# Kernel optimization log

Measured on AMD Instinct MI355X. Metric: run time of the kernel, lower is better.

## Reference

```python
import jax, jax.numpy as jnp
import numpy as np

B, T, H = 16, 1024, 256
L = 2048
NUM_CLASSES = 100000

def setup_inputs() -> dict:
    key = jax.random.key(0)
    k1, k2, k3 = jax.random.split(key, 3)
    inputs = jax.random.normal(k1, (B, T, H), dtype=jnp.float32)
    labels_selected = jax.random.randint(k2, (B, L), 0, NUM_CLASSES + 1, dtype=jnp.int64)
    attention_table = jax.random.normal(k3, (NUM_CLASSES + 1, H), dtype=jnp.float32) * 0.02
    return {"inputs": inputs, "labels_selected": labels_selected, "attention_table": attention_table}

def reference(inputs, labels_selected, attention_table):
    # Gather label embeddings as queries: (B, L, H)
    attn_weights = attention_table[labels_selected]
    # Unscaled dot-product scores: (B, L, T)
    scores = jnp.einsum('blh,bth->blt', attn_weights, inputs)
    attention = jax.nn.softmax(scores, axis=-1)
    # Weighted sum of inputs: (B, L, H)
    logits = jnp.einsum('blt,bth->blh', attention, inputs)
    return (logits, attention)
```

## Files before the change

kernel.cpp:

```cpp
#include <hip/hip_runtime.h>

#define Bdim 16
#define Tdim 1024
#define Hdim 256
#define Ldim 2048

typedef __attribute__((ext_vector_type(8))) short short8;
typedef __attribute__((ext_vector_type(4))) short short4_t;
typedef __attribute__((ext_vector_type(16))) float floatx16;

__device__ __forceinline__ ushort f2bf(float x) {
    union { float f; unsigned u; } v; v.f = x;
    unsigned r = v.u + 0x7fffu + ((v.u >> 16) & 1u);
    return (ushort)(r >> 16);
}
__device__ __forceinline__ float bf2f(ushort u) {
    union { unsigned u; float f; } v; v.u = ((unsigned)u) << 16;
    return v.f;
}
__device__ __forceinline__ short8 pack8(float4 a, float4 b) {
    short8 r;
    r[0] = (short)f2bf(a.x); r[1] = (short)f2bf(a.y); r[2] = (short)f2bf(a.z); r[3] = (short)f2bf(a.w);
    r[4] = (short)f2bf(b.x); r[5] = (short)f2bf(b.y); r[6] = (short)f2bf(b.z); r[7] = (short)f2bf(b.w);
    return r;
}

__global__ __launch_bounds__(256) void convert_kernel(
    const float* __restrict__ in, ushort* __restrict__ outN, ushort* __restrict__ outT) {
    __shared__ ushort lds[64][68];
    const int b = blockIdx.z, h0 = blockIdx.y * 64, t0 = blockIdx.x * 64;
    const int tid = threadIdx.x;
#pragma unroll
    for (int i = 0; i < 2; i++) {
        const int tt = tid + i * 256;
        const int r = tt >> 3, c = (tt & 7) * 8;
        const float4* src = (const float4*)(in + ((size_t)(b * Tdim + t0 + r)) * Hdim + h0 + c);
        short8 u = pack8(src[0], src[1]);
        *(short8*)(outN + ((size_t)(b * Tdim + t0 + r)) * Hdim + h0 + c) = u;
        short4_t lo = {u[0], u[1], u[2], u[3]}, hi = {u[4], u[5], u[6], u[7]};
        *(short4_t*)&lds[r][c] = lo;
        *(short4_t*)&lds[r][c + 4] = hi;
    }
    __syncthreads();
#pragma unroll
    for (int i = 0; i < 2; i++) {
        const int tt = tid + i * 256;
        const int hh = tt >> 3, c = (tt & 7) * 8;
        short8 u;
#pragma unroll
        for (int j = 0; j < 8; j++) u[j] = (short)lds[c + j][hh];
        *(short8*)(outT + ((size_t)(b * Hdim + h0 + hh)) * Tdim + t0 + c) = u;
    }
}

__global__ __launch_bounds__(512, 4) void attn_kernel(
    const float* __restrict__ table, const int* __restrict__ labels,
    const ushort* __restrict__ kn, const ushort* __restrict__ vt,
    float* __restrict__ logits_out, float* __restrict__ attn_out) {
    __shared__ ushort P[32][1032];
    __shared__ float stats[8][32];
    float* rowinv = &stats[0][0];

    const int bid = blockIdx.x;
    const int xcd = bid & 7, w = bid >> 3;
    const int b = xcd * 2 + (w >> 6);
    const int l0 = (w & 63) * 32;
    const int tid = threadIdx.x;
    const int wave = tid >> 6, lane = tid & 63;
    const int half = lane >> 5, m = lane & 31;

    ushort (*qt)[264] = (ushort(*)[264]) & P[0][0];

    {
        const int row = tid >> 4, cc = (tid & 15) * 16;
        const int lab = labels[b * Ldim + l0 + row];
        const float4* src = (const float4*)(table + (size_t)lab * Hdim + cc);
        float4 f0 = src[0], f1 = src[1], f2 = src[2], f3 = src[3];
        *(short8*)&qt[row][cc] = pack8(f0, f1);
        *(short8*)&qt[row][cc + 8] = pack8(f2, f3);
    }
    __syncthreads();

    floatx16 acc[4];
#pragma unroll
    for (int nt = 0; nt < 4; nt++)
#pragma unroll
        for (int r = 0; r < 16; r++) acc[nt][r] = 0.f;
    {
        const int t0s = wave * 128;
        const ushort* kb = kn + ((size_t)(b * Tdim + t0s + m)) * Hdim + half * 8;
        const ushort* qb = &qt[m][half * 8];
#pragma unroll
        for (int ks = 0; ks < 16; ks++) {
            short8 af = *(const short8*)(qb + ks * 16);
            short8 b0 = *(const short8*)(kb + ks * 16);
            short8 b1 = *(const short8*)(kb + 32 * Hdim + ks * 16);
            short8 b2 = *(const short8*)(kb + 64 * Hdim + ks * 16);
            short8 b3 = *(const short8*)(kb + 96 * Hdim + ks * 16);
            acc[0] = __builtin_amdgcn_mfma_f32_32x32x16_bf16(af, b0, acc[0], 0, 0, 0);
            acc[1] = __builtin_amdgcn_mfma_f32_32x32x16_bf16(af, b1, acc[1], 0, 0, 0);
            acc[2] = __builtin_amdgcn_mfma_f32_32x32x16_bf16(af, b2, acc[2], 0, 0, 0);
            acc[3] = __builtin_amdgcn_mfma_f32_32x32x16_bf16(af, b3, acc[3], 0, 0, 0);
        }
    }

    float rs[16];
#pragma unroll
    for (int nt = 0; nt < 4; nt++)
#pragma unroll
        for (int r = 0; r < 16; r++) {
            float e = __expf(acc[nt][r]);
            acc[nt][r] = e;
            if (nt == 0) rs[r] = e; else rs[r] += e;
        }
#pragma unroll
    for (int s = 1; s < 32; s <<= 1)
#pragma unroll
        for (int r = 0; r < 16; r++) rs[r] += __shfl_xor(rs[r], s, 64);
    if (m == 0) {
#pragma unroll
        for (int r = 0; r < 16; r++) stats[wave][(r & 3) + 8 * (r >> 2) + 4 * half] = rs[r];
    }
    __syncthreads();

    {
        const int t0s = wave * 128;
#pragma unroll
        for (int nt = 0; nt < 4; nt++)
#pragma unroll
            for (int r = 0; r < 16; r++)
                P[(r & 3) + 8 * (r >> 2) + 4 * half][t0s + nt * 32 + m] = f2bf(acc[nt][r]);
    }
    if (tid < 32) {
        float d = 0.f;
#pragma unroll
        for (int wv = 0; wv < 8; wv++) d += stats[wv][tid];
        rowinv[tid] = 1.0f / d;
    }

    const int h0 = wave * 32;
    const ushort* vb = vt + ((size_t)(b * Hdim + h0 + m)) * Tdim + half * 8;
    short8 v0p = *(const short8*)(vb);
    short8 v1p = *(const short8*)(vb + 32 * 16);
    __syncthreads();

#pragma unroll
    for (int r = 0; r < 4; r++) {
        const int row = wave * 4 + r;
        const float inv = rowinv[row];
        const ushort* pr = &P[row][lane * 8];
        float* dst = attn_out + ((size_t)(b * Ldim + l0 + row)) * Tdim + lane * 8;
        short8 u0 = *(const short8*)(pr);
        short8 u1 = *(const short8*)(pr + 512);
        float4 o;
        o.x = bf2f((ushort)u0[0]) * inv; o.y = bf2f((ushort)u0[1]) * inv;
        o.z = bf2f((ushort)u0[2]) * inv; o.w = bf2f((ushort)u0[3]) * inv;
        *(float4*)(dst) = o;
        o.x = bf2f((ushort)u0[4]) * inv; o.y = bf2f((ushort)u0[5]) * inv;
        o.z = bf2f((ushort)u0[6]) * inv; o.w = bf2f((ushort)u0[7]) * inv;
        *(float4*)(dst + 4) = o;
        o.x = bf2f((ushort)u1[0]) * inv; o.y = bf2f((ushort)u1[1]) * inv;
        o.z = bf2f((ushort)u1[2]) * inv; o.w = bf2f((ushort)u1[3]) * inv;
        *(float4*)(dst + 512) = o;
        o.x = bf2f((ushort)u1[4]) * inv; o.y = bf2f((ushort)u1[5]) * inv;
        o.z = bf2f((ushort)u1[6]) * inv; o.w = bf2f((ushort)u1[7]) * inv;
        *(float4*)(dst + 516) = o;
    }

    {
        floatx16 c0, c1;
#pragma unroll
        for (int r = 0; r < 16; r++) { c0[r] = 0.f; c1[r] = 0.f; }
        const ushort* pb = &P[m][half * 8];
#pragma unroll
        for (int ks = 0; ks < 32; ks++) {
            short8 a0 = *(const short8*)(pb + ks * 16);
            short8 v0 = (ks == 0) ? v0p : *(const short8*)(vb + ks * 16);
            c0 = __builtin_amdgcn_mfma_f32_32x32x16_bf16(a0, v0, c0, 0, 0, 0);
            short8 a1 = *(const short8*)(pb + (ks + 32) * 16);
            short8 v1 = (ks == 0) ? v1p : *(const short8*)(vb + (ks + 32) * 16);
            c1 = __builtin_amdgcn_mfma_f32_32x32x16_bf16(a1, v1, c1, 0, 0, 0);
        }
#pragma unroll
        for (int r = 0; r < 16; r++) {
            const int row = (r & 3) + 8 * (r >> 2) + 4 * half;
            logits_out[((size_t)(b * Ldim + l0 + row)) * Hdim + h0 + m] =
                (c0[r] + c1[r]) * rowinv[row];
        }
    }
}

extern "C" void kernel_launch(void* const* d_in, const int* in_sizes, int n_in,
                              void* d_out, int out_size, void* d_ws, size_t ws_size,
                              hipStream_t stream) {
    const float* inputs = (const float*)d_in[0];
    const int* labels   = (const int*)d_in[1];
    const float* table  = (const float*)d_in[2];
    float* out = (float*)d_out;

    ushort* kn = (ushort*)d_ws;
    ushort* vt = kn + (size_t)Bdim * Tdim * Hdim;

    convert_kernel<<<dim3(Tdim / 64, Hdim / 64, Bdim), 256, 0, stream>>>(inputs, kn, vt);

    float* logits_out = out;
    float* attn_out = out + (size_t)Bdim * Ldim * Hdim;
    attn_kernel<<<Bdim * (Ldim / 32), 512, 0, stream>>>(table, labels, kn, vt,
                                                        logits_out, attn_out);
}
```

Measured before the change: 356.1 us.

## Stream P through double-buffered 256-column LDS strips and store attention from registers

Replaces the full 32x1032 bf16 probability tile in LDS with two 32x264 strip buffers that are filled in turn by pairs of waves, with a barrier between strips, during the P·V MFMA loop. The attention output is now written straight from registers (packed bf16 times the row inverse) instead of being re-read from LDS. The aim is to cut LDS use per block so more blocks fit per CU, and to remove the LDS round trip for the attention store. In exchange the kernel has more barriers, holds the packed values in extra registers, and the per-lane strided float stores of attention are less coalesced than the old float4 row writes.

```diff
diff --git a/kernel.cpp b/kernel.cpp
--- a/kernel.cpp
+++ b/kernel.cpp
@@ -57,7 +57,7 @@
     const float* __restrict__ table, const int* __restrict__ labels,
     const ushort* __restrict__ kn, const ushort* __restrict__ vt,
     float* __restrict__ logits_out, float* __restrict__ attn_out) {
-    __shared__ ushort P[32][1032];
+    __shared__ ushort bufs[2][32][264];
     __shared__ float stats[8][32];
     float* rowinv = &stats[0][0];
 
@@ -69,7 +69,7 @@
     const int wave = tid >> 6, lane = tid & 63;
     const int half = lane >> 5, m = lane & 31;
 
-    ushort (*qt)[264] = (ushort(*)[264]) & P[0][0];
+    ushort (*qt)[264] = bufs[0];
 
     {
         const int row = tid >> 4, cc = (tid & 15) * 16;
@@ -123,14 +123,6 @@
     }
     __syncthreads();
 
-    {
-        const int t0s = wave * 128;
-#pragma unroll
-        for (int nt = 0; nt < 4; nt++)
-#pragma unroll
-            for (int r = 0; r < 16; r++)
-                P[(r & 3) + 8 * (r >> 2) + 4 * half][t0s + nt * 32 + m] = f2bf(acc[nt][r]);
-    }
     if (tid < 32) {
         float d = 0.f;
 #pragma unroll
@@ -138,48 +130,68 @@
         rowinv[tid] = 1.0f / d;
     }
 
-    const int h0 = wave * 32;
-    const ushort* vb = vt + ((size_t)(b * Hdim + h0 + m)) * Tdim + half * 8;
-    short8 v0p = *(const short8*)(vb);
-    short8 v1p = *(const short8*)(vb + 32 * 16);
-    __syncthreads();
-
-#pragma unroll
-    for (int r = 0; r < 4; r++) {
-        const int row = wave * 4 + r;
-        const float inv = rowinv[row];
-        const ushort* pr = &P[row][lane * 8];
-        float* dst = attn_out + ((size_t)(b * Ldim + l0 + row)) * Tdim + lane * 8;
-        short8 u0 = *(const short8*)(pr);
-        short8 u1 = *(const short8*)(pr + 512);
-        float4 o;
-        o.x = bf2f((ushort)u0[0]) * inv; o.y = bf2f((ushort)u0[1]) * inv;
-        o.z = bf2f((ushort)u0[2]) * inv; o.w = bf2f((ushort)u0[3]) * inv;
-        *(float4*)(dst) = o;
-        o.x = bf2f((ushort)u0[4]) * inv; o.y = bf2f((ushort)u0[5]) * inv;
-        o.z = bf2f((ushort)u0[6]) * inv; o.w = bf2f((ushort)u0[7]) * inv;
-        *(float4*)(dst + 4) = o;
-        o.x = bf2f((ushort)u1[0]) * inv; o.y = bf2f((ushort)u1[1]) * inv;
-        o.z = bf2f((ushort)u1[2]) * inv; o.w = bf2f((ushort)u1[3]) * inv;
-        *(float4*)(dst + 512) = o;
-        o.x = bf2f((ushort)u1[4]) * inv; o.y = bf2f((ushort)u1[5]) * inv;
-        o.z = bf2f((ushort)u1[6]) * inv; o.w = bf2f((ushort)u1[7]) * inv;
-        *(float4*)(dst + 516) = o;
+    unsigned pk[2][16];
+#pragma unroll
+    for (int p = 0; p < 2; p++)
+#pragma unroll
+        for (int r = 0; r < 16; r++)
+            pk[p][r] = (unsigned)f2bf(acc[2 * p][r]) |
+                       ((unsigned)f2bf(acc[2 * p + 1][r]) << 16);
+
+    const int coff = (wave & 1) * 128;
+    auto write_strip = [&](int bi) {
+        ushort(*dst)[264] = bufs[bi];
+#pragma unroll
+        for (int p = 0; p < 2; p++)
+#pragma unroll
+            for (int r = 0; r < 16; r++) {
+                const int row = (r & 3) + 8 * (r >> 2) + 4 * half;
+                dst[row][coff + (2 * p) * 32 + m] = (ushort)(pk[p][r] & 0xffffu);
+                dst[row][coff + (2 * p + 1) * 32 + m] = (ushort)(pk[p][r] >> 16);
+            }
+    };
+
+    if ((wave >> 1) == 0) write_strip(0);
+    __syncthreads();
+
+    {
+        float inv[16];
+#pragma unroll
+        for (int r = 0; r < 16; r++) inv[r] = rowinv[(r & 3) + 8 * (r >> 2) + 4 * half];
+        float* dst = attn_out + ((size_t)(b * Ldim + l0)) * Tdim + wave * 128 + m;
+#pragma unroll
+        for (int p = 0; p < 2; p++)
+#pragma unroll
+            for (int r = 0; r < 16; r++) {
+                const int row = (r & 3) + 8 * (r >> 2) + 4 * half;
+                dst[(size_t)row * Tdim + (2 * p) * 32] =
+                    bf2f((ushort)(pk[p][r] & 0xffffu)) * inv[r];
+                dst[(size_t)row * Tdim + (2 * p + 1) * 32] =
+                    bf2f((ushort)(pk[p][r] >> 16)) * inv[r];
+            }
     }
 
     {
         floatx16 c0, c1;
 #pragma unroll
         for (int r = 0; r < 16; r++) { c0[r] = 0.f; c1[r] = 0.f; }
-        const ushort* pb = &P[m][half * 8];
-#pragma unroll
-        for (int ks = 0; ks < 32; ks++) {
-            short8 a0 = *(const short8*)(pb + ks * 16);
-            short8 v0 = (ks == 0) ? v0p : *(const short8*)(vb + ks * 16);
-            c0 = __builtin_amdgcn_mfma_f32_32x32x16_bf16(a0, v0, c0, 0, 0, 0);
-            short8 a1 = *(const short8*)(pb + (ks + 32) * 16);
-            short8 v1 = (ks == 0) ? v1p : *(const short8*)(vb + (ks + 32) * 16);
-            c1 = __builtin_amdgcn_mfma_f32_32x32x16_bf16(a1, v1, c1, 0, 0, 0);
+        const int h0 = wave * 32;
+        const ushort* vb = vt + ((size_t)(b * Hdim + h0 + m)) * Tdim + half * 8;
+#pragma unroll
+        for (int c = 0; c < 4; c++) {
+            if (c) __syncthreads();
+            if (c < 3 && (wave >> 1) == c + 1) write_strip((c + 1) & 1);
+            const ushort* pb = &bufs[c & 1][m][half * 8];
+            const ushort* vc = vb + c * 256;
+#pragma unroll
+            for (int ks = 0; ks < 8; ks++) {
+                short8 a0 = *(const short8*)(pb + (2 * ks) * 16);
+                short8 v0 = *(const short8*)(vc + (2 * ks) * 16);
+                c0 = __builtin_amdgcn_mfma_f32_32x32x16_bf16(a0, v0, c0, 0, 0, 0);
+                short8 a1 = *(const short8*)(pb + (2 * ks + 1) * 16);
+                short8 v1 = *(const short8*)(vc + (2 * ks + 1) * 16);
+                c1 = __builtin_amdgcn_mfma_f32_32x32x16_bf16(a1, v1, c1, 0, 0, 0);
+            }
         }
 #pragma unroll
         for (int r = 0; r < 16; r++) {
```

Result: no change. 350.5 us (-1.6%).
